# Kernel tuning notes

Hardware: AMD Instinct MI355X
Metric: run time of the kernel (lower is better)

## Reference

```python
import jax, jax.numpy as jnp
import numpy as np

B, T, NQ, NK = 2, 8, 128, 128
DIM_IN, DIM_OUT = 64, 256


def setup_inputs() -> dict:
    key = jax.random.key(0)
    ks = jax.random.split(key, 6)
    scale = 0.05  # keep tanh out of full saturation
    return {
        "query": jax.random.normal(ks[0], (B, NQ, DIM_IN), dtype=jnp.float32),
        "keys": jax.random.normal(ks[1], (B, T, NK, DIM_IN), dtype=jnp.float32),
        "Wq": jax.random.normal(ks[2], (DIM_IN, DIM_OUT), dtype=jnp.float32) * scale,
        "Wk": jax.random.normal(ks[3], (DIM_IN, DIM_OUT), dtype=jnp.float32) * scale,
        "bk": jax.random.normal(ks[4], (DIM_OUT,), dtype=jnp.float32) * scale,
        "v": jax.random.normal(ks[5], (DIM_OUT,), dtype=jnp.float32) * scale,
    }


def reference(query, keys, Wq, Wk, bk, v):
    # q: [B, Nq, D], k: [B, T, Nk, D]
    q = jnp.einsum("bqi,id->bqd", query, Wq)
    k = jnp.einsum("btki,id->btkd", keys, Wk) + bk
    # broadcast add -> [B, T, Nq, Nk, D], tanh, then score projection D->1
    h = jnp.tanh(q[:, None, :, None, :] + k[:, :, None, :, :])
    scores = jnp.einsum("btqkd,d->btqk", h, v)
    return jax.nn.softmax(scores, axis=-1)
```

## Files before the change

kernel.cpp:

```cpp
#include <hip/hip_runtime.h>

#define C_TANH 2.8853900817779268f

__global__ __launch_bounds__(256) void qproj_kernel(
    const float* __restrict__ query, const float* __restrict__ Wq,
    float* __restrict__ q1) {
  int row = blockIdx.x;
  int d   = threadIdx.x;
  __shared__ float qrow[64];
  if (d < 64) qrow[d] = query[row * 64 + d];
  __syncthreads();
  float acc = 0.f;
#pragma unroll
  for (int i = 0; i < 64; ++i) acc += qrow[i] * Wq[i * 256 + d];
  q1[row * 256 + d] = acc * C_TANH;
}

__global__ __launch_bounds__(128) void kproj_kernel(
    const float* __restrict__ keys, const float* __restrict__ Wk,
    const float* __restrict__ bk, float* __restrict__ k2) {
  int bid = blockIdx.x;
  int bt  = bid >> 8;
  int d   = bid & 255;
  int k   = threadIdx.x;
  const float* krow = keys + (bt * 128 + k) * 64;
  float acc = bk[d];
#pragma unroll
  for (int i = 0; i < 64; ++i) acc += krow[i] * Wk[i * 256 + d];
  k2[(bt * 256 + d) * 128 + k] = acc * C_TANH;
}

__global__ __launch_bounds__(256) void score_kernel(
    const float* __restrict__ q1, const float* __restrict__ v,
    const float* __restrict__ k2, float* __restrict__ out) {
  __shared__ float2 qv[2][256];
  __shared__ float redm[4], reds[4];
  int tid = threadIdx.x;
  int r   = tid >> 7;
  int k   = tid & 127;
  int wid = tid >> 6;
  int g0  = blockIdx.x * 2;
  int bt  = g0 >> 7;
  int b   = g0 >> 10;
  int q1base = b * 128 + (g0 & 127);

  for (int idx = tid; idx < 512; idx += 256) {
    int r2 = idx >> 8;
    int d  = idx & 255;
    qv[r2][d] = make_float2(q1[(q1base + r2) * 256 + d], v[d]);
  }
  __syncthreads();

  const float* kp = k2 + bt * 256 * 128 + k;
  float acc = 0.f;
#pragma unroll 8
  for (int d = 0; d < 256; ++d) {
    float2 t = qv[r][d];
    float x  = t.x + kp[d * 128];
    float e  = __builtin_amdgcn_exp2f(x);
    acc += t.y * __builtin_amdgcn_rcpf(1.0f + e);
  }
  float s = -C_TANH * acc;

  float m = s;
#pragma unroll
  for (int off = 32; off > 0; off >>= 1) m = fmaxf(m, __shfl_xor(m, off, 64));
  if ((tid & 63) == 0) redm[wid] = m;
  __syncthreads();
  float rowm = fmaxf(redm[r * 2], redm[r * 2 + 1]);

  float e = __builtin_amdgcn_exp2f(s - rowm);
  float ssum = e;
#pragma unroll
  for (int off = 32; off > 0; off >>= 1) ssum += __shfl_xor(ssum, off, 64);
  if ((tid & 63) == 0) reds[wid] = ssum;
  __syncthreads();
  float tot = reds[r * 2] + reds[r * 2 + 1];

  out[(g0 + r) * 128 + k] = e * __builtin_amdgcn_rcpf(tot);
}

extern "C" void kernel_launch(void* const* d_in, const int* in_sizes, int n_in,
                              void* d_out, int out_size, void* d_ws, size_t ws_size,
                              hipStream_t stream) {
  const float* query = (const float*)d_in[0];
  const float* keys  = (const float*)d_in[1];
  const float* Wq    = (const float*)d_in[2];
  const float* Wk    = (const float*)d_in[3];
  const float* bk    = (const float*)d_in[4];
  const float* v     = (const float*)d_in[5];
  float* out = (float*)d_out;

  float* ws = (float*)d_ws;
  float* q1 = ws;
  float* k2 = ws + 65536;

  qproj_kernel<<<256, 256, 0, stream>>>(query, Wq, q1);
  kproj_kernel<<<4096, 128, 0, stream>>>(keys, Wk, bk, k2);
  score_kernel<<<1024, 256, 0, stream>>>(q1, v, k2, out);
}
```

Before: 103.7 us.

## Fuse query projection into score kernel and retile key projection for Wk reuse

Removes the separate query-projection kernel: each score block now computes its two projected query rows from query and Wq directly, which saves one launch and the q1 round trip through global memory. The cost is redundant work, since each query row is recomputed by every time step that uses it, eight times in total. The key projection is restructured so each block stages 8 key rows in shared memory and each thread accumulates 8 outputs per Wk load. That cuts the grid from 4096 to 256 blocks and reuses Wk across keys, but the k2 stores become strided per thread.

```diff
diff --git a/kernel.cpp b/kernel.cpp
--- a/kernel.cpp
+++ b/kernel.cpp
@@ -2,38 +2,51 @@
 
 #define C_TANH 2.8853900817779268f
 
-__global__ __launch_bounds__(256) void qproj_kernel(
-    const float* __restrict__ query, const float* __restrict__ Wq,
-    float* __restrict__ q1) {
-  int row = blockIdx.x;
-  int d   = threadIdx.x;
-  __shared__ float qrow[64];
-  if (d < 64) qrow[d] = query[row * 64 + d];
-  __syncthreads();
-  float acc = 0.f;
-#pragma unroll
-  for (int i = 0; i < 64; ++i) acc += qrow[i] * Wq[i * 256 + d];
-  q1[row * 256 + d] = acc * C_TANH;
-}
-
-__global__ __launch_bounds__(128) void kproj_kernel(
+__global__ __launch_bounds__(256) void kproj_kernel(
     const float* __restrict__ keys, const float* __restrict__ Wk,
     const float* __restrict__ bk, float* __restrict__ k2) {
   int bid = blockIdx.x;
-  int bt  = bid >> 8;
-  int d   = bid & 255;
-  int k   = threadIdx.x;
-  const float* krow = keys + (bt * 128 + k) * 64;
-  float acc = bk[d];
+  int bt  = bid >> 4;
+  int kg  = bid & 15;
+  int d   = threadIdx.x;
+  __shared__ float4 krows4[128];
+
+  if (threadIdx.x < 128)
+    krows4[threadIdx.x] =
+        ((const float4*)(keys + bt * 8192 + kg * 512))[threadIdx.x];
+  __syncthreads();
+
+  float acc[8];
+  float bias = bk[d];
 #pragma unroll
-  for (int i = 0; i < 64; ++i) acc += krow[i] * Wk[i * 256 + d];
-  k2[(bt * 256 + d) * 128 + k] = acc * C_TANH;
+  for (int kk = 0; kk < 8; ++kk) acc[kk] = bias;
+
+#pragma unroll 4
+  for (int i4 = 0; i4 < 16; ++i4) {
+    float wa = Wk[(i4 * 4 + 0) * 256 + d];
+    float wb = Wk[(i4 * 4 + 1) * 256 + d];
+    float wc = Wk[(i4 * 4 + 2) * 256 + d];
+    float wd = Wk[(i4 * 4 + 3) * 256 + d];
+#pragma unroll
+    for (int kk = 0; kk < 8; ++kk) {
+      float4 kr = krows4[kk * 16 + i4];
+      acc[kk] = fmaf(kr.x, wa, acc[kk]);
+      acc[kk] = fmaf(kr.y, wb, acc[kk]);
+      acc[kk] = fmaf(kr.z, wc, acc[kk]);
+      acc[kk] = fmaf(kr.w, wd, acc[kk]);
+    }
+  }
+#pragma unroll
+  for (int kk = 0; kk < 8; ++kk)
+    k2[(bt * 256 + d) * 128 + kg * 8 + kk] = acc[kk] * C_TANH;
 }
 
 __global__ __launch_bounds__(256) void score_kernel(
-    const float* __restrict__ q1, const float* __restrict__ v,
-    const float* __restrict__ k2, float* __restrict__ out) {
+    const float* __restrict__ query, const float* __restrict__ Wq,
+    const float* __restrict__ v, const float* __restrict__ k2,
+    float* __restrict__ out) {
   __shared__ float2 qv[2][256];
+  __shared__ float qrow[2][64];
   __shared__ float redm[4], reds[4];
   int tid = threadIdx.x;
   int r   = tid >> 7;
@@ -42,12 +55,18 @@
   int g0  = blockIdx.x * 2;
   int bt  = g0 >> 7;
   int b   = g0 >> 10;
-  int q1base = b * 128 + (g0 & 127);
+  int q0  = b * 128 + (g0 & 127);
+
+  if (tid < 128) qrow[tid >> 6][tid & 63] = query[q0 * 64 + tid];
+  __syncthreads();
 
   for (int idx = tid; idx < 512; idx += 256) {
-    int r2 = idx >> 8;
+    int rr = idx >> 8;
     int d  = idx & 255;
-    qv[r2][d] = make_float2(q1[(q1base + r2) * 256 + d], v[d]);
+    float acc = 0.f;
+#pragma unroll
+    for (int i = 0; i < 64; ++i) acc += qrow[rr][i] * Wq[i * 256 + d];
+    qv[rr][d] = make_float2(acc * C_TANH, v[d]);
   }
   __syncthreads();
 
@@ -91,11 +110,8 @@
   const float* v     = (const float*)d_in[5];
   float* out = (float*)d_out;
 
-  float* ws = (float*)d_ws;
-  float* q1 = ws;
-  float* k2 = ws + 65536;
+  float* k2 = (float*)d_ws;
 
-  qproj_kernel<<<256, 256, 0, stream>>>(query, Wq, q1);
-  kproj_kernel<<<4096, 128, 0, stream>>>(keys, Wk, bk, k2);
-  score_kernel<<<1024, 256, 0, stream>>>(q1, v, k2, out);
+  kproj_kernel<<<256, 256, 0, stream>>>(keys, Wk, bk, k2);
+  score_kernel<<<1024, 256, 0, stream>>>(query, Wq, v, k2, out);
 }
```

New measurement: 91.60 us. 11.6% less time.
